# Performance work log

Measured on AMD Instinct MI355X. Metric: run time of the kernel, lower is better.

Reference implementation:

```python
import jax, jax.numpy as jnp
import numpy as np

B, C, MID, OUT, T, N = 8, 128, 64, 128, 4, 512


def setup_inputs() -> dict:
    key = jax.random.key(0)
    ks = jax.random.split(key, 5)
    def w(k, o, i, scale):
        return (jax.random.normal(k, (o, i), jnp.float32) * scale)
    return {
        "pc": jax.random.normal(ks[0], (B, C, T, N), jnp.float32),
        "theta_w": w(ks[1], MID, C, 0.05), "theta_b": jnp.zeros((MID,), jnp.float32),
        "phi_w": w(ks[2], MID, C, 0.05), "phi_b": jnp.zeros((MID,), jnp.float32),
        "g_w": w(ks[3], MID, C, 0.05), "g_b": jnp.zeros((MID,), jnp.float32),
        "refine_w": w(ks[4], OUT, MID, 0.05), "refine_b": jnp.zeros((OUT,), jnp.float32),
    }


def reference(pc, theta_w, theta_b, phi_w, phi_b, g_w, g_b, refine_w, refine_b):
    b, c, t, n = pc.shape
    tn = t * n
    # pt_utils.Conv2d with bn=False: 1x1 conv + bias + ReLU
    def proj(wt, bs):
        h = jnp.einsum('oc,bctn->botn', wt, pc) + bs[None, :, None, None]
        return jax.nn.relu(h).reshape(b, -1, tn)  # [B, mid, TN]

    theta = proj(theta_w, theta_b).transpose(0, 2, 1)  # [B, TN, mid]
    phi = proj(phi_w, phi_b)                            # [B, mid, TN]
    g = proj(g_w, g_b).transpose(0, 2, 1)               # [B, TN, mid]

    scores = jnp.einsum('bqm,bmk->bqk', theta, phi)     # [B, TN, TN]
    corr = jax.nn.softmax(scores, axis=1)               # softmax over QUERY axis (dim=1)
    y = jnp.einsum('bqk,bkm->bmq', corr, g)             # bmm then transpose(1,2): [B, mid, TN]

    # pt_utils.Conv1d with bn=False: 1x1 conv + bias + ReLU
    refined = jax.nn.relu(jnp.einsum('om,bmq->boq', refine_w, y) + refine_b[None, :, None])
    # faithful raw reshape (row-major, same as torch) then permute, plus residual
    z = refined.reshape(b, t, n, -1).transpose(0, 3, 1, 2) + pc
    return z
```

## Files before the change

### kernel.cpp

```cpp
#include <hip/hip_runtime.h>


constexpr int NL75_TN  = 2048;
constexpr int NL75_MID = 64;
constexpr int NL75_C   = 128;
constexpr float NL75_L2E = 1.4426950408889634f;

typedef __attribute__((ext_vector_type(8))) short nl75_bf8;
typedef __attribute__((ext_vector_type(4))) float nl75_f4;

__device__ __forceinline__ unsigned short nl75_f2b(float f) {
  unsigned x = __float_as_uint(f);
  return (unsigned short)((x + 0x7fffu + ((x >> 16) & 1u)) >> 16);
}

__device__ __forceinline__ unsigned int nl75_pkbf16(float lo, float hi) {
  unsigned int r;
  asm("v_cvt_pk_bf16_f32 %0, %1, %2" : "=v"(r) : "v"(lo), "v"(hi));
  return r;
}

__device__ __forceinline__ float nl75_exp2(float x) {
  float r;
  asm("v_exp_f32 %0, %1" : "=v"(r) : "v"(x));
  return r;
}

typedef const __attribute__((address_space(1))) unsigned int* nl75_gp;
typedef __attribute__((address_space(3))) unsigned int* nl75_lp;
__device__ __forceinline__ void nl75_gld16(const void* g, void* l) {
  __builtin_amdgcn_global_load_lds((nl75_gp)g, (nl75_lp)l, 16, 0, 0);
}

__device__ __forceinline__ void nl75_stage64(const unsigned short* src,
                                             size_t pitch, unsigned short* lds,
                                             int tid) {
  const int w = tid >> 6, lane = tid & 63;
#pragma unroll
  for (int r = 0; r < 2; r++) {
    const int slot = r * 256 + w * 64 + lane;
    const int row = slot >> 3, x = slot & 7;
    const unsigned short* s =
        src + (size_t)row * pitch + ((x * 8) ^ ((row & 7) << 3));
    nl75_gld16(s, lds + (size_t)(r * 256 + w * 64) * 8);
  }
}

__global__ void NonLocalLayer_75771813036638_kernel() {}

__global__ void nl75_proj(const float* pc, const float* w0, const float* b0,
                          const float* w1, const float* b1, const float* w2,
                          const float* b2, unsigned short* thT,
                          unsigned short* phT, unsigned short* gN, int bOff,
                          int nb) {
  __shared__ float wT[NL75_C][68];
  const int bl = blockIdx.x, pj = blockIdx.y, qt = blockIdx.z;
  const int b = bOff + bl;
  const float* wp = (pj == 0) ? w0 : (pj == 1) ? w1 : w2;
  const float* bp = (pj == 0) ? b0 : (pj == 1) ? b1 : b2;
  const int tid = threadIdx.x;
  for (int i = tid; i < NL75_MID * NL75_C; i += 256)
    wT[i & 127][i >> 7] = wp[i];
  __syncthreads();
  const int lq = tid & 63, mg = tid >> 6;
  const int q = qt * 64 + lq, m0 = mg * 16;
  const float* pcb = pc + (long long)b * NL75_C * NL75_TN + q;
  float acc[16];
#pragma unroll
  for (int i = 0; i < 16; i++) acc[i] = bp[m0 + i];
  for (int c = 0; c < NL75_C; c++) {
    float p = pcb[(long long)c * NL75_TN];
#pragma unroll
    for (int i = 0; i < 16; i++) acc[i] = fmaf(wT[c][m0 + i], p, acc[i]);
  }
  if (pj < 2) {
    unsigned int u[8];
#pragma unroll
    for (int i = 0; i < 8; i++)
      u[i] = nl75_pkbf16(fmaxf(acc[2 * i], 0.0f), fmaxf(acc[2 * i + 1], 0.0f));
    unsigned short* dst =
        (pj == 0 ? thT : phT) + ((size_t)bl * NL75_TN + q) * 64 + m0;
    *reinterpret_cast<uint4*>(dst) = *reinterpret_cast<uint4*>(&u[0]);
    *reinterpret_cast<uint4*>(dst + 8) = *reinterpret_cast<uint4*>(&u[4]);
  } else {
#pragma unroll
    for (int i = 0; i < 16; i++)
      gN[((size_t)bl * NL75_MID + m0 + i) * NL75_TN + q] =
          nl75_f2b(fmaxf(acc[i], 0.0f));
  }
}

__global__ void nl75_stats(const unsigned short* thT, const unsigned short* phT,
                           float* Mp, float* Sp, int nb, int qsplit) {
  __shared__ unsigned short thL[2][64 * 64];
  const int bl = blockIdx.x;
  const int kt = blockIdx.y & 31, qs = blockIdx.y >> 5;
  const int tid = threadIdx.x, lane = tid & 63, w = tid >> 6;
  const int l15 = lane & 15, quad = lane >> 4;
  const int k0 = kt * 64;
  const unsigned short* thB = thT + (size_t)bl * NL75_TN * 64;
  const unsigned short* phB = phT + (size_t)bl * NL75_TN * 64;
  const size_t kr = (size_t)(k0 + w * 16 + l15) * 64;
  const nl75_bf8 b0 = *(const nl75_bf8*)&phB[kr + quad * 8];
  const nl75_bf8 b1 = *(const nl75_bf8*)&phB[kr + 32 + quad * 8];
  const int qtN = 32 / qsplit, qtBeg = qs * qtN;
  nl75_stage64(thB + (size_t)(qtBeg * 64) * 64, 64, thL[0], tid);
  __syncthreads();
  float M = -1e30f, S = 0.0f;
  for (int qt = qtBeg; qt < qtBeg + qtN; qt++) {
    const int cur = (qt - qtBeg) & 1;
    if (qt + 1 < qtBeg + qtN)
      nl75_stage64(thB + (size_t)((qt + 1) * 64) * 64, 64, thL[cur ^ 1], tid);
    __builtin_amdgcn_s_setprio(1);
#pragma unroll
    for (int q16 = 0; q16 < 4; q16++) {
      const int qr = q16 * 16 + l15;
      const int sw = (qr & 7) << 3;
      const nl75_bf8 a0 = *(const nl75_bf8*)&thL[cur][qr * 64 + ((quad * 8) ^ sw)];
      const nl75_bf8 a1 =
          *(const nl75_bf8*)&thL[cur][qr * 64 + ((32 + quad * 8) ^ sw)];
      nl75_f4 c = {0.0f, 0.0f, 0.0f, 0.0f};
      c = __builtin_amdgcn_mfma_f32_16x16x32_bf16(a0, b0, c, 0, 0, 0);
      c = __builtin_amdgcn_mfma_f32_16x16x32_bf16(a1, b1, c, 0, 0, 0);
      float mx = fmaxf(fmaxf(c[0], c[1]), fmaxf(c[2], c[3]));
      float nM = fmaxf(M, mx);
      float sum = __expf(c[0] - nM) + __expf(c[1] - nM) + __expf(c[2] - nM) +
                  __expf(c[3] - nM);
      S = S * __expf(M - nM) + sum;
      M = nM;
    }
    __builtin_amdgcn_s_setprio(0);
    __syncthreads();
  }
#pragma unroll
  for (int off = 16; off <= 32; off <<= 1) {
    float Mo = __shfl_xor(M, off);
    float So = __shfl_xor(S, off);
    float nM = fmaxf(M, Mo);
    S = S * __expf(M - nM) + So * __expf(Mo - nM);
    M = nM;
  }
  if (quad == 0) {
    const long long base = ((long long)(qs * nb + bl)) * NL75_TN + k0;
    Mp[base + w * 16 + l15] = M;
    Sp[base + w * 16 + l15] = S;
  }
}

__global__ void nl75_sred(const float* Mp, const float* Sp, float* ekW, int nb,
                          int qsplit) {
  const int bl = blockIdx.x;
  const int k = blockIdx.y * 256 + threadIdx.x;
  float M = -1e30f;
  for (int qs = 0; qs < qsplit; qs++)
    M = fmaxf(M, Mp[((size_t)(qs * nb + bl)) * NL75_TN + k]);
  float S = 0.0f;
  for (int qs = 0; qs < qsplit; qs++) {
    size_t idx = ((size_t)(qs * nb + bl)) * NL75_TN + k;
    S += Sp[idx] * __expf(Mp[idx] - M);
  }
  ekW[(size_t)bl * NL75_TN + k] = M * NL75_L2E + __log2f(S);
}

__global__ void nl75_attn(const unsigned short* thT, const unsigned short* phT,
                          const unsigned short* gN, const float* ekW,
                          float* yPart, int nb, int ksplit) {
  __shared__ unsigned short phL[2][64 * 64];
  __shared__ unsigned short gL[2][64 * 64];
  const int wg = blockIdx.x;
  const int bl = wg % nb;
  const int rest = wg / nb;
  const int qt = rest & 15, ks = rest >> 4;
  const int tid = threadIdx.x, lane = tid & 63, w = tid >> 6;
  const int l15 = lane & 15, quad = lane >> 4;
  const int q0 = qt * 128;
  const unsigned short* thB = thT + (size_t)bl * NL75_TN * 64;
  const unsigned short* phB = phT + (size_t)bl * NL75_TN * 64;
  const unsigned short* gB = gN + (size_t)bl * NL75_MID * NL75_TN;
  const float* ekB = ekW + (size_t)bl * NL75_TN;
  const int ktN = 32 / ksplit;
  const int ktBeg = ks * ktN, ktEnd = ktBeg + ktN;
  nl75_stage64(phB + (size_t)(ktBeg * 64) * 64, 64, phL[0], tid);
  nl75_stage64(gB + ktBeg * 64, NL75_TN, gL[0], tid);
  nl75_bf8 aq[2][2];
#pragma unroll
  for (int s = 0; s < 2; s++) {
    const size_t qr = (size_t)(q0 + s * 64 + w * 16 + l15) * 64;
    aq[s][0] = *(const nl75_bf8*)&thB[qr + quad * 8];
    aq[s][1] = *(const nl75_bf8*)&thB[qr + 32 + quad * 8];
  }
  nl75_f4 yacc[2][4];
#pragma unroll
  for (int s = 0; s < 2; s++)
#pragma unroll
    for (int i = 0; i < 4; i++) yacc[s][i] = (nl75_f4){0.0f, 0.0f, 0.0f, 0.0f};
  __syncthreads();
  union Frag { nl75_bf8 h; unsigned int u[4]; };
  for (int kt = ktBeg; kt < ktEnd; kt++) {
    const int cur = (kt - ktBeg) & 1;
    const int k0 = kt * 64;
    if (kt + 1 < ktEnd) {
      nl75_stage64(phB + (size_t)((kt + 1) * 64) * 64, 64, phL[cur ^ 1], tid);
      nl75_stage64(gB + (kt + 1) * 64, NL75_TN, gL[cur ^ 1], tid);
    }
    nl75_f4 ek[4];
#pragma unroll
    for (int t = 0; t < 4; t++)
      ek[t] = *(const nl75_f4*)&ekB[k0 + t * 16 + quad * 4];
    __builtin_amdgcn_s_setprio(1);
    unsigned int pk[2][8];
#pragma unroll
    for (int t = 0; t < 4; t++) {
      const int krr = t * 16 + l15;
      const int sw = (krr & 7) << 3;
      const nl75_bf8 b0 =
          *(const nl75_bf8*)&phL[cur][krr * 64 + ((quad * 8) ^ sw)];
      const nl75_bf8 b1 =
          *(const nl75_bf8*)&phL[cur][krr * 64 + ((32 + quad * 8) ^ sw)];
#pragma unroll
      for (int s = 0; s < 2; s++) {
        nl75_f4 c = {0.0f, 0.0f, 0.0f, 0.0f};
        c = __builtin_amdgcn_mfma_f32_16x16x32_bf16(b0, aq[s][0], c, 0, 0, 0);
        c = __builtin_amdgcn_mfma_f32_16x16x32_bf16(b1, aq[s][1], c, 0, 0, 0);
        pk[s][t * 2 + 0] =
            nl75_pkbf16(nl75_exp2(fmaf(c[0], NL75_L2E, -ek[t][0])),
                        nl75_exp2(fmaf(c[1], NL75_L2E, -ek[t][1])));
        pk[s][t * 2 + 1] =
            nl75_pkbf16(nl75_exp2(fmaf(c[2], NL75_L2E, -ek[t][2])),
                        nl75_exp2(fmaf(c[3], NL75_L2E, -ek[t][3])));
      }
    }
#pragma unroll
    for (int mtile = 0; mtile < 4; mtile++) {
      const int m = mtile * 16 + l15;
      const int sw = (m & 7) << 3;
      const unsigned short* row = &gL[cur][m * 64];
      Frag bg0, bg1;
      *(uint2*)&bg0.u[0] = *(const uint2*)&row[(quad * 4) ^ sw];
      *(uint2*)&bg0.u[2] = *(const uint2*)&row[(16 + quad * 4) ^ sw];
      *(uint2*)&bg1.u[0] = *(const uint2*)&row[(32 + quad * 4) ^ sw];
      *(uint2*)&bg1.u[2] = *(const uint2*)&row[(48 + quad * 4) ^ sw];
#pragma unroll
      for (int s = 0; s < 2; s++) {
        Frag a0, a1;
        a0.u[0] = pk[s][0]; a0.u[1] = pk[s][1];
        a0.u[2] = pk[s][2]; a0.u[3] = pk[s][3];
        a1.u[0] = pk[s][4]; a1.u[1] = pk[s][5];
        a1.u[2] = pk[s][6]; a1.u[3] = pk[s][7];
        yacc[s][mtile] = __builtin_amdgcn_mfma_f32_16x16x32_bf16(
            a0.h, bg0.h, yacc[s][mtile], 0, 0, 0);
        yacc[s][mtile] = __builtin_amdgcn_mfma_f32_16x16x32_bf16(
            a1.h, bg1.h, yacc[s][mtile], 0, 0, 0);
      }
    }
    __builtin_amdgcn_s_setprio(0);
    __syncthreads();
  }
  float* yB = yPart + ((size_t)(ks * nb + bl) * NL75_MID) * NL75_TN;
#pragma unroll
  for (int s = 0; s < 2; s++)
#pragma unroll
    for (int mtile = 0; mtile < 4; mtile++) {
      float4 v = make_float4(yacc[s][mtile][0], yacc[s][mtile][1],
                             yacc[s][mtile][2], yacc[s][mtile][3]);
      *(float4*)&yB[(size_t)(mtile * 16 + l15) * NL75_TN + q0 + s * 64 +
                    w * 16 + quad * 4] = v;
    }
}

__global__ void nl75_yred(const float* yPart, float* y, int nb, int ksplit) {
  const size_t tot = (size_t)nb * NL75_MID * NL75_TN / 4;
  const size_t stride = tot;
  const float4* src = (const float4*)yPart;
  float4* dst = (float4*)y;
  for (size_t i = (size_t)blockIdx.x * 256 + threadIdx.x; i < tot;
       i += (size_t)gridDim.x * 256) {
    float4 a = src[i];
    for (int ks = 1; ks < ksplit; ks++) {
      float4 b = src[(size_t)ks * stride + i];
      a.x += b.x; a.y += b.y; a.z += b.z; a.w += b.w;
    }
    dst[i] = a;
  }
}

__global__ void nl75_refsc(const float* yIn, const float* rW, const float* rB,
                           const float* pc, float* outP, int bOff, int nb,
                           int ksplit) {
  __shared__ float rwS[32][66];
  __shared__ float yS[NL75_MID][132];
  const int bl = blockIdx.x, cg = blockIdx.y, t = blockIdx.z;
  const int b = bOff + bl, c0 = cg * 8, tid = threadIdx.x;
  for (int i = tid; i < 32 * NL75_MID; i += 256) {
    int oh = i >> 6, m = i & 63;
    rwS[oh][m] = rW[(long long)(t * 32 + oh) * NL75_MID + m];
  }
  if (ksplit == 1) {
    const float* yB0 = yIn + (size_t)bl * NL75_MID * NL75_TN;
    for (int i = tid; i < NL75_MID * 32; i += 256) {
      int m = i >> 5, r = i & 31;
      int i16 = r >> 1, half = r & 1;
      const float4 v = *(const float4*)&yB0[(size_t)m * NL75_TN + i16 * 128 +
                                            c0 + half * 4];
      *(float4*)&yS[m][i16 * 8 + half * 4] = v;
    }
  } else {
    for (int i = tid; i < NL75_MID * 128; i += 256) {
      int m = i >> 7, qi = i & 127;
      int i16 = qi >> 3, cl = qi & 7;
      long long off = (long long)m * NL75_TN + i16 * 128 + c0 + cl;
      float v = 0.0f;
      for (int ks = 0; ks < ksplit; ks++)
        v += yIn[((long long)(ks * nb + bl) * NL75_MID) * NL75_TN + off];
      yS[m][qi] = v;
    }
  }
  __syncthreads();
  const int oh0 = (tid >> 5) * 4;
  const int q4 = (tid & 31) * 4;
  float acc[4][4];
#pragma unroll
  for (int i = 0; i < 4; i++) {
    float bias = rB[t * 32 + oh0 + i];
#pragma unroll
    for (int j = 0; j < 4; j++) acc[i][j] = bias;
  }
  for (int m = 0; m < NL75_MID; m++) {
    float yv[4];
#pragma unroll
    for (int j = 0; j < 4; j++) yv[j] = yS[m][q4 + j];
#pragma unroll
    for (int i = 0; i < 4; i++) {
      float w = rwS[oh0 + i][m];
#pragma unroll
      for (int j = 0; j < 4; j++) acc[i][j] = fmaf(w, yv[j], acc[i][j]);
    }
  }
  __syncthreads();
  float* outS = &yS[0][0];
  const int NP = 516;
#pragma unroll
  for (int i = 0; i < 4; i++) {
    const int oh = oh0 + i;
#pragma unroll
    for (int j = 0; j < 4; j++) {
      const int qi = q4 + j;
      outS[(qi & 7) * NP + oh * 16 + (qi >> 3)] = fmaxf(acc[i][j], 0.0f);
    }
  }
  __syncthreads();
  const size_t obase = (((size_t)b * 128 + c0) * 4 + t) * 512;
#pragma unroll
  for (int ii = 0; ii < 4; ii++) {
    const int fi = ii * 256 + tid;
    const int cl = fi >> 7, n0 = (fi & 127) * 4;
    float4 v = *(const float4*)&outS[cl * NP + n0];
    const size_t gi = obase + (size_t)cl * 4 * 512 + n0;
    const float4 p = *(const float4*)&pc[gi];
    v.x += p.x; v.y += p.y; v.z += p.z; v.w += p.w;
    *(float4*)&outP[gi] = v;
  }
}

extern "C" void kernel_launch(void* const* d_in, const int* in_sizes, int n_in,
                              void* d_out, int out_size, void* d_ws, size_t ws_size,
                              hipStream_t stream) {
  const float* pc = (const float*)d_in[0];
  const float* tw = (const float*)d_in[1];
  const float* tb = (const float*)d_in[2];
  const float* pw = (const float*)d_in[3];
  const float* pb = (const float*)d_in[4];
  const float* gw = (const float*)d_in[5];
  const float* gb = (const float*)d_in[6];
  const float* rw = (const float*)d_in[7];
  const float* rb = (const float*)d_in[8];
  float* out = (float*)d_out;

  const size_t yPB = (size_t)NL75_MID * NL75_TN;
  const size_t bfB8 = 3ull * 8 * NL75_TN * 64 * 2;
  const size_t base8 = bfB8 + 2ull * 8 * NL75_TN * 4;
  auto need = [&](int qs, int ks, int yr) -> size_t {
    return base8 + (2ull * qs * 8 * NL75_TN + (size_t)ks * 8 * yPB +
                    (size_t)yr * 8 * yPB) * 4;
  };
  const size_t needMid = base8 + 8ull * yPB * 4;

  int nb, qsplit, ksplit;
  bool alias, yred;
  if (ws_size >= need(8, 8, 1)) {
    nb = 8; qsplit = 8; ksplit = 8; alias = false; yred = true;
  } else if (ws_size >= need(8, 4, 1)) {
    nb = 8; qsplit = 8; ksplit = 4; alias = false; yred = true;
  } else if (ws_size >= need(4, 4, 1)) {
    nb = 8; qsplit = 4; ksplit = 4; alias = false; yred = true;
  } else if (ws_size >= need(4, 4, 0)) {
    nb = 8; qsplit = 4; ksplit = 4; alias = false; yred = false;
  } else if (ws_size >= needMid) {
    nb = 8; qsplit = 1; ksplit = 1; alias = true; yred = false;
  } else {
    nb = 1; qsplit = 1; ksplit = 1; alias = true; yred = false;
  }
  const int nloop = 8 / nb;

  unsigned short* thT = (unsigned short*)d_ws;
  unsigned short* phT = thT + (size_t)nb * NL75_TN * 64;
  unsigned short* gN = phT + (size_t)nb * NL75_TN * 64;
  float* s1 = (float*)(gN + (size_t)nb * NL75_MID * NL75_TN);
  float* ekW = s1 + (size_t)nb * NL75_TN;
  float *Mp, *Sp, *yPart, *yFull;
  if (alias) {
    Mp = s1; Sp = ekW;
    yPart = ekW + (size_t)nb * NL75_TN;
    yFull = yPart;
  } else {
    Mp = ekW + (size_t)nb * NL75_TN;
    Sp = Mp + (size_t)qsplit * nb * NL75_TN;
    yPart = Sp + (size_t)qsplit * nb * NL75_TN;
    yFull = yPart + (size_t)ksplit * nb * yPB;
  }

  for (int l = 0; l < nloop; l++) {
    const int bOff = l * nb;
    nl75_proj<<<dim3(nb, 3, 32), 256, 0, stream>>>(pc, tw, tb, pw, pb, gw, gb,
                                                   thT, phT, gN, bOff, nb);
    nl75_stats<<<dim3(nb, 32 * qsplit), 256, 0, stream>>>(thT, phT, Mp, Sp,
                                                          nb, qsplit);
    nl75_sred<<<dim3(nb, 8), 256, 0, stream>>>(Mp, Sp, ekW, nb, qsplit);
    nl75_attn<<<dim3(16 * ksplit * nb), 256, 0, stream>>>(thT, phT, gN, ekW,
                                                          yPart, nb, ksplit);
    if (yred) {
      nl75_yred<<<dim3(1024), 256, 0, stream>>>(yPart, yFull, nb, ksplit);
      nl75_refsc<<<dim3(nb, 16, 4), 256, 0, stream>>>(yFull, rw, rb, pc, out,
                                                      bOff, nb, 1);
    } else {
      nl75_refsc<<<dim3(nb, 16, 4), 256, 0, stream>>>(yPart, rw, rb, pc, out,
                                                      bOff, nb, ksplit);
    }
  }
}
```

Measured before the change: 144.2 us.

## Replace key-split attention with full-key 64-query tiles and drop y reduction

The attention kernel no longer splits the key dimension across workgroups. Each workgroup now handles 64 queries over all 2048 keys, and the grid becomes 32*nb blocks instead of 16*ksplit*nb. This removes the partial-y buffers and the separate nl75_yred reduction launch, which cuts global traffic and one launch. The cost is fewer workgroups (256 vs up to 1024), a longer serial loop per block, and phi/g tiles staged once per 64 queries instead of per 128, so there is less reuse.

```diff
diff --git a/kernel.cpp b/kernel.cpp
--- a/kernel.cpp
+++ b/kernel.cpp
@@ -164,42 +164,36 @@
 
 __global__ void nl75_attn(const unsigned short* thT, const unsigned short* phT,
                           const unsigned short* gN, const float* ekW,
-                          float* yPart, int nb, int ksplit) {
+                          float* yOut, int nb) {
   __shared__ unsigned short phL[2][64 * 64];
   __shared__ unsigned short gL[2][64 * 64];
   const int wg = blockIdx.x;
   const int bl = wg % nb;
-  const int rest = wg / nb;
-  const int qt = rest & 15, ks = rest >> 4;
+  const int qt = wg / nb;
   const int tid = threadIdx.x, lane = tid & 63, w = tid >> 6;
   const int l15 = lane & 15, quad = lane >> 4;
-  const int q0 = qt * 128;
+  const int q0 = qt * 64;
   const unsigned short* thB = thT + (size_t)bl * NL75_TN * 64;
   const unsigned short* phB = phT + (size_t)bl * NL75_TN * 64;
   const unsigned short* gB = gN + (size_t)bl * NL75_MID * NL75_TN;
   const float* ekB = ekW + (size_t)bl * NL75_TN;
-  const int ktN = 32 / ksplit;
-  const int ktBeg = ks * ktN, ktEnd = ktBeg + ktN;
-  nl75_stage64(phB + (size_t)(ktBeg * 64) * 64, 64, phL[0], tid);
-  nl75_stage64(gB + ktBeg * 64, NL75_TN, gL[0], tid);
-  nl75_bf8 aq[2][2];
-#pragma unroll
-  for (int s = 0; s < 2; s++) {
-    const size_t qr = (size_t)(q0 + s * 64 + w * 16 + l15) * 64;
-    aq[s][0] = *(const nl75_bf8*)&thB[qr + quad * 8];
-    aq[s][1] = *(const nl75_bf8*)&thB[qr + 32 + quad * 8];
-  }
-  nl75_f4 yacc[2][4];
-#pragma unroll
-  for (int s = 0; s < 2; s++)
-#pragma unroll
-    for (int i = 0; i < 4; i++) yacc[s][i] = (nl75_f4){0.0f, 0.0f, 0.0f, 0.0f};
+  nl75_stage64(phB, 64, phL[0], tid);
+  nl75_stage64(gB, NL75_TN, gL[0], tid);
+  nl75_bf8 aq0, aq1;
+  {
+    const size_t qr = (size_t)(q0 + w * 16 + l15) * 64;
+    aq0 = *(const nl75_bf8*)&thB[qr + quad * 8];
+    aq1 = *(const nl75_bf8*)&thB[qr + 32 + quad * 8];
+  }
+  nl75_f4 yacc[4];
+#pragma unroll
+  for (int i = 0; i < 4; i++) yacc[i] = (nl75_f4){0.0f, 0.0f, 0.0f, 0.0f};
   __syncthreads();
   union Frag { nl75_bf8 h; unsigned int u[4]; };
-  for (int kt = ktBeg; kt < ktEnd; kt++) {
-    const int cur = (kt - ktBeg) & 1;
+  for (int kt = 0; kt < 32; kt++) {
+    const int cur = kt & 1;
     const int k0 = kt * 64;
-    if (kt + 1 < ktEnd) {
+    if (kt + 1 < 32) {
       nl75_stage64(phB + (size_t)((kt + 1) * 64) * 64, 64, phL[cur ^ 1], tid);
       nl75_stage64(gB + (kt + 1) * 64, NL75_TN, gL[cur ^ 1], tid);
     }
@@ -208,7 +202,7 @@
     for (int t = 0; t < 4; t++)
       ek[t] = *(const nl75_f4*)&ekB[k0 + t * 16 + quad * 4];
     __builtin_amdgcn_s_setprio(1);
-    unsigned int pk[2][8];
+    unsigned int pk[8];
 #pragma unroll
     for (int t = 0; t < 4; t++) {
       const int krr = t * 16 + l15;
@@ -217,19 +211,17 @@
           *(const nl75_bf8*)&phL[cur][krr * 64 + ((quad * 8) ^ sw)];
       const nl75_bf8 b1 =
           *(const nl75_bf8*)&phL[cur][krr * 64 + ((32 + quad * 8) ^ sw)];
-#pragma unroll
-      for (int s = 0; s < 2; s++) {
-        nl75_f4 c = {0.0f, 0.0f, 0.0f, 0.0f};
-        c = __builtin_amdgcn_mfma_f32_16x16x32_bf16(b0, aq[s][0], c, 0, 0, 0);
-        c = __builtin_amdgcn_mfma_f32_16x16x32_bf16(b1, aq[s][1], c, 0, 0, 0);
-        pk[s][t * 2 + 0] =
-            nl75_pkbf16(nl75_exp2(fmaf(c[0], NL75_L2E, -ek[t][0])),
-                        nl75_exp2(fmaf(c[1], NL75_L2E, -ek[t][1])));
-        pk[s][t * 2 + 1] =
-            nl75_pkbf16(nl75_exp2(fmaf(c[2], NL75_L2E, -ek[t][2])),
-                        nl75_exp2(fmaf(c[3], NL75_L2E, -ek[t][3])));
-      }
-    }
+      nl75_f4 c = {0.0f, 0.0f, 0.0f, 0.0f};
+      c = __builtin_amdgcn_mfma_f32_16x16x32_bf16(b0, aq0, c, 0, 0, 0);
+      c = __builtin_amdgcn_mfma_f32_16x16x32_bf16(b1, aq1, c, 0, 0, 0);
+      pk[t * 2 + 0] = nl75_pkbf16(nl75_exp2(fmaf(c[0], NL75_L2E, -ek[t][0])),
+                                  nl75_exp2(fmaf(c[1], NL75_L2E, -ek[t][1])));
+      pk[t * 2 + 1] = nl75_pkbf16(nl75_exp2(fmaf(c[2], NL75_L2E, -ek[t][2])),
+                                  nl75_exp2(fmaf(c[3], NL75_L2E, -ek[t][3])));
+    }
+    Frag a0, a1;
+    a0.u[0] = pk[0]; a0.u[1] = pk[1]; a0.u[2] = pk[2]; a0.u[3] = pk[3];
+    a1.u[0] = pk[4]; a1.u[1] = pk[5]; a1.u[2] = pk[6]; a1.u[3] = pk[7];
 #pragma unroll
     for (int mtile = 0; mtile < 4; mtile++) {
       const int m = mtile * 16 + l15;
@@ -240,47 +232,21 @@
       *(uint2*)&bg0.u[2] = *(const uint2*)&row[(16 + quad * 4) ^ sw];
       *(uint2*)&bg1.u[0] = *(const uint2*)&row[(32 + quad * 4) ^ sw];
       *(uint2*)&bg1.u[2] = *(const uint2*)&row[(48 + quad * 4) ^ sw];
-#pragma unroll
-      for (int s = 0; s < 2; s++) {
-        Frag a0, a1;
-        a0.u[0] = pk[s][0]; a0.u[1] = pk[s][1];
-        a0.u[2] = pk[s][2]; a0.u[3] = pk[s][3];
-        a1.u[0] = pk[s][4]; a1.u[1] = pk[s][5];
-        a1.u[2] = pk[s][6]; a1.u[3] = pk[s][7];
-        yacc[s][mtile] = __builtin_amdgcn_mfma_f32_16x16x32_bf16(
-            a0.h, bg0.h, yacc[s][mtile], 0, 0, 0);
-        yacc[s][mtile] = __builtin_amdgcn_mfma_f32_16x16x32_bf16(
-            a1.h, bg1.h, yacc[s][mtile], 0, 0, 0);
-      }
+      yacc[mtile] = __builtin_amdgcn_mfma_f32_16x16x32_bf16(a0.h, bg0.h,
+                                                            yacc[mtile], 0, 0, 0);
+      yacc[mtile] = __builtin_amdgcn_mfma_f32_16x16x32_bf16(a1.h, bg1.h,
+                                                            yacc[mtile], 0, 0, 0);
     }
     __builtin_amdgcn_s_setprio(0);
     __syncthreads();
   }
-  float* yB = yPart + ((size_t)(ks * nb + bl) * NL75_MID) * NL75_TN;
-#pragma unroll
-  for (int s = 0; s < 2; s++)
-#pragma unroll
-    for (int mtile = 0; mtile < 4; mtile++) {
-      float4 v = make_float4(yacc[s][mtile][0], yacc[s][mtile][1],
-                             yacc[s][mtile][2], yacc[s][mtile][3]);
-      *(float4*)&yB[(size_t)(mtile * 16 + l15) * NL75_TN + q0 + s * 64 +
-                    w * 16 + quad * 4] = v;
-    }
-}
-
-__global__ void nl75_yred(const float* yPart, float* y, int nb, int ksplit) {
-  const size_t tot = (size_t)nb * NL75_MID * NL75_TN / 4;
-  const size_t stride = tot;
-  const float4* src = (const float4*)yPart;
-  float4* dst = (float4*)y;
-  for (size_t i = (size_t)blockIdx.x * 256 + threadIdx.x; i < tot;
-       i += (size_t)gridDim.x * 256) {
-    float4 a = src[i];
-    for (int ks = 1; ks < ksplit; ks++) {
-      float4 b = src[(size_t)ks * stride + i];
-      a.x += b.x; a.y += b.y; a.z += b.z; a.w += b.w;
-    }
-    dst[i] = a;
+  float* yB = yOut + (size_t)bl * NL75_MID * NL75_TN;
+#pragma unroll
+  for (int mtile = 0; mtile < 4; mtile++) {
+    float4 v = make_float4(yacc[mtile][0], yacc[mtile][1], yacc[mtile][2],
+                           yacc[mtile][3]);
+    *(float4*)&yB[(size_t)(mtile * 16 + l15) * NL75_TN + q0 + w * 16 +
+                  quad * 4] = v;
   }
 }
 
@@ -377,47 +343,25 @@
   float* out = (float*)d_out;
 
   const size_t yPB = (size_t)NL75_MID * NL75_TN;
-  const size_t bfB8 = 3ull * 8 * NL75_TN * 64 * 2;
-  const size_t base8 = bfB8 + 2ull * 8 * NL75_TN * 4;
-  auto need = [&](int qs, int ks, int yr) -> size_t {
-    return base8 + (2ull * qs * 8 * NL75_TN + (size_t)ks * 8 * yPB +
-                    (size_t)yr * 8 * yPB) * 4;
+  auto need = [&](int nb, int qs) -> size_t {
+    return (3ull * nb * NL75_TN * 64 * 2) +
+           ((size_t)nb * NL75_TN + 2ull * qs * nb * NL75_TN +
+            (size_t)nb * yPB) * 4;
   };
-  const size_t needMid = base8 + 8ull * yPB * 4;
-
-  int nb, qsplit, ksplit;
-  bool alias, yred;
-  if (ws_size >= need(8, 8, 1)) {
-    nb = 8; qsplit = 8; ksplit = 8; alias = false; yred = true;
-  } else if (ws_size >= need(8, 4, 1)) {
-    nb = 8; qsplit = 8; ksplit = 4; alias = false; yred = true;
-  } else if (ws_size >= need(4, 4, 1)) {
-    nb = 8; qsplit = 4; ksplit = 4; alias = false; yred = true;
-  } else if (ws_size >= need(4, 4, 0)) {
-    nb = 8; qsplit = 4; ksplit = 4; alias = false; yred = false;
-  } else if (ws_size >= needMid) {
-    nb = 8; qsplit = 1; ksplit = 1; alias = true; yred = false;
-  } else {
-    nb = 1; qsplit = 1; ksplit = 1; alias = true; yred = false;
-  }
+
+  int nb, qsplit;
+  if (ws_size >= need(8, 8))      { nb = 8; qsplit = 8; }
+  else if (ws_size >= need(8, 1)) { nb = 8; qsplit = 1; }
+  else                            { nb = 1; qsplit = 1; }
   const int nloop = 8 / nb;
 
   unsigned short* thT = (unsigned short*)d_ws;
   unsigned short* phT = thT + (size_t)nb * NL75_TN * 64;
   unsigned short* gN = phT + (size_t)nb * NL75_TN * 64;
-  float* s1 = (float*)(gN + (size_t)nb * NL75_MID * NL75_TN);
-  float* ekW = s1 + (size_t)nb * NL75_TN;
-  float *Mp, *Sp, *yPart, *yFull;
-  if (alias) {
-    Mp = s1; Sp = ekW;
-    yPart = ekW + (size_t)nb * NL75_TN;
-    yFull = yPart;
-  } else {
-    Mp = ekW + (size_t)nb * NL75_TN;
-    Sp = Mp + (size_t)qsplit * nb * NL75_TN;
-    yPart = Sp + (size_t)qsplit * nb * NL75_TN;
-    yFull = yPart + (size_t)ksplit * nb * yPB;
-  }
+  float* ekW = (float*)(gN + (size_t)nb * NL75_MID * NL75_TN);
+  float* Mp = ekW + (size_t)nb * NL75_TN;
+  float* Sp = Mp + (size_t)qsplit * nb * NL75_TN;
+  float* yFull = Sp + (size_t)qsplit * nb * NL75_TN;
 
   for (int l = 0; l < nloop; l++) {
     const int bOff = l * nb;
@@ -426,15 +370,8 @@
     nl75_stats<<<dim3(nb, 32 * qsplit), 256, 0, stream>>>(thT, phT, Mp, Sp,
                                                           nb, qsplit);
     nl75_sred<<<dim3(nb, 8), 256, 0, stream>>>(Mp, Sp, ekW, nb, qsplit);
-    nl75_attn<<<dim3(16 * ksplit * nb), 256, 0, stream>>>(thT, phT, gN, ekW,
-                                                          yPart, nb, ksplit);
-    if (yred) {
-      nl75_yred<<<dim3(1024), 256, 0, stream>>>(yPart, yFull, nb, ksplit);
-      nl75_refsc<<<dim3(nb, 16, 4), 256, 0, stream>>>(yFull, rw, rb, pc, out,
-                                                      bOff, nb, 1);
-    } else {
-      nl75_refsc<<<dim3(nb, 16, 4), 256, 0, stream>>>(yPart, rw, rb, pc, out,
-                                                      bOff, nb, ksplit);
-    }
-  }
-}
+    nl75_attn<<<dim3(32 * nb), 256, 0, stream>>>(thT, phT, gN, ekW, yFull, nb);
+    nl75_refsc<<<dim3(nb, 16, 4), 256, 0, stream>>>(yFull, rw, rb, pc, out,
+                                                    bOff, nb, 1);
+  }
+}
```

Result: slower. 158.0 us (+9.5%).
